# Kernel optimization log

Hardware: AMD Instinct MI355X
Metric: run time of the kernel (lower is better)

The kernel has to match this reference:

```python
import jax, jax.numpy as jnp
import numpy as np

WH, WW = 14, 14
NUM_HEADS = 12
NUM_REL = (2 * WH - 1) * (2 * WW - 1) + 3  # 732


def _gen_rel_pos_index(wh, ww):
    # Faithful numpy port of gen_relative_position_index (static, host-side)
    area = wh * ww
    coords = np.stack(np.meshgrid(np.arange(wh), np.arange(ww), indexing='ij'))  # (2, wh, ww)
    cf = coords.reshape(2, -1)  # (2, area)
    rel = cf[:, :, None] - cf[:, None, :]  # (2, area, area)
    rel = rel.transpose(1, 2, 0).copy()  # (area, area, 2)
    rel[..., 0] += wh - 1
    rel[..., 1] += ww - 1
    rel[..., 0] *= 2 * ww - 1
    nrd = (2 * wh - 1) * (2 * ww - 1) + 3
    idx = np.zeros((area + 1, area + 1), dtype=np.int64)
    idx[1:, 1:] = rel.sum(-1)
    idx[0, 0:] = nrd - 3
    idx[0:, 0] = nrd - 2
    idx[0, 0] = nrd - 1
    return idx


REL_IDX = jnp.asarray(_gen_rel_pos_index(WH, WW))  # (197, 197) int


def setup_inputs() -> dict:
    key = jax.random.key(0)
    k0, k1, k2, k3 = jax.random.split(key, 4)
    B, N, C = 64, WH * WW + 1, 768
    x = jax.random.normal(k0, (B, N, C), jnp.float32)
    qkv_w = jax.random.normal(k1, (3 * C, C), jnp.float32) * 0.02
    q_bias = jnp.zeros((C,), jnp.float32)
    k_bias = jnp.zeros((C,), jnp.float32)  # non-trainable buffer, always zeros
    v_bias = jnp.zeros((C,), jnp.float32)
    rel_table = jax.random.normal(k2, (NUM_REL, NUM_HEADS), jnp.float32) * 0.02
    proj_w = jax.random.normal(k3, (C, C), jnp.float32) * 0.02
    proj_b = jnp.zeros((C,), jnp.float32)
    return {"x": x, "qkv_w": qkv_w, "q_bias": q_bias, "k_bias": k_bias,
            "v_bias": v_bias, "rel_table": rel_table, "proj_w": proj_w, "proj_b": proj_b}


def reference(x, qkv_w, q_bias, k_bias, v_bias, rel_table, proj_w, proj_b):
    B, N, C = x.shape
    H = NUM_HEADS
    D = C // H
    scale = D ** -0.5
    # fused qkv projection with concatenated (q, k(zero), v) bias
    qkv_bias = jnp.concatenate([q_bias, k_bias, v_bias])
    qkv = x @ qkv_w.T + qkv_bias  # (B, N, 3C)
    qkv = qkv.reshape(B, N, 3, H, D).transpose(2, 0, 3, 1, 4)  # (3, B, H, N, D)
    q, k, v = qkv[0], qkv[1], qkv[2]
    # scores + gathered relative position bias
    attn = jnp.einsum('bhnd,bhmd->bhnm', q * scale, k)  # (B, H, N, N)
    rpb = rel_table[REL_IDX].transpose(2, 0, 1)  # (H, N, N)
    attn = jax.nn.softmax(attn + rpb[None], axis=-1)
    out = jnp.einsum('bhnm,bhmd->bhnd', attn, v)  # (B, H, N, D)
    out = out.transpose(0, 2, 1, 3).reshape(B, N, C)
    return out @ proj_w.T + proj_b
```

## Files before the change

kernel.cpp:

```cpp
#include <hip/hip_runtime.h>
#include <math.h>

#define B_   64
#define N_   197
#define C_   768
#define H_   12
#define D_   64
#define BN   12608
#define BN_PAD 12672
#define QKV_ELEMS 9682944
#define SCALE 0.125f
#define STRV 80

typedef unsigned short ushort_t;
using bf16x8  = __attribute__((ext_vector_type(8))) __bf16;
using floatx4 = __attribute__((ext_vector_type(4))) float;
using ushort8 = __attribute__((ext_vector_type(8))) unsigned short;

__device__ __forceinline__ ushort_t f2bf(float f) {
    union { float f; unsigned u; } v; v.f = f;
    unsigned r = v.u + 0x7FFF + ((v.u >> 16) & 1);
    return (ushort_t)(r >> 16);
}

__device__ __forceinline__ void gload_lds16(const void* g, void* l) {
    __builtin_amdgcn_global_load_lds(
        (const __attribute__((address_space(1))) unsigned*)g,
        (__attribute__((address_space(3))) unsigned*)l, 16, 0, 0);
}

__global__ __launch_bounds__(256) void cvt_f32_bf16(
    const float* __restrict__ src, ushort_t* __restrict__ dst, int n4)
{
    int i = blockIdx.x * 256 + threadIdx.x;
    if (i < n4) {
        float4 v = ((const float4*)src)[i];
        ushort4 o;
        o.x = f2bf(v.x); o.y = f2bf(v.y); o.z = f2bf(v.z); o.w = f2bf(v.w);
        ((ushort4*)dst)[i] = o;
    }
}

__global__ __launch_bounds__(256, 4) void qkv_gemm_mfma(
    const ushort_t* __restrict__ xb,
    const ushort_t* __restrict__ wb,
    const float* __restrict__ qb,
    const float* __restrict__ kb,
    const float* __restrict__ vb,
    ushort_t* __restrict__ qkvb)
{
    __shared__ ushort_t lA[128 * 64];
    __shared__ ushort_t lB[128 * 64];
    const int t = threadIdx.x;
    const int w = t >> 6, lane = t & 63;
    const int quad = lane >> 4, li = lane & 15;
    const int wm = w >> 1, wn = w & 1;
    const int o0 = blockIdx.x * 128, m0 = blockIdx.y * 128;

    floatx4 acc[4][4];
#pragma unroll
    for (int i = 0; i < 4; ++i)
#pragma unroll
        for (int j = 0; j < 4; ++j) acc[i][j] = (floatx4)0.f;

    const int rloc = lane >> 3;
    const int gdma = (lane & 7) ^ rloc;
    const int rx   = li & 7;

    for (int kt = 0; kt < 12; ++kt) {
        const int k0 = kt * 64;
#pragma unroll
        for (int s = 0; s < 4; ++s) {
            const int rb = w * 32 + s * 8;
            gload_lds16(xb + ((size_t)(m0 + rb + rloc)) * 768 + k0 + gdma * 8,
                        &lA[rb * 64]);
            gload_lds16(wb + ((size_t)(o0 + rb + rloc)) * 768 + k0 + gdma * 8,
                        &lB[rb * 64]);
        }
        __syncthreads();
#pragma unroll
        for (int kk = 0; kk < 2; ++kk) {
            bf16x8 af[4], bfr[4];
#pragma unroll
            for (int mi = 0; mi < 4; ++mi)
                af[mi] = *(const bf16x8*)
                    &lA[(wm * 64 + mi * 16 + li) * 64 + ((kk * 4 + quad) ^ rx) * 8];
#pragma unroll
            for (int ni = 0; ni < 4; ++ni)
                bfr[ni] = *(const bf16x8*)
                    &lB[(wn * 64 + ni * 16 + li) * 64 + ((kk * 4 + quad) ^ rx) * 8];
#pragma unroll
            for (int mi = 0; mi < 4; ++mi)
#pragma unroll
                for (int ni = 0; ni < 4; ++ni)
                    acc[mi][ni] = __builtin_amdgcn_mfma_f32_16x16x32_bf16(
                        af[mi], bfr[ni], acc[mi][ni], 0, 0, 0);
        }
        __syncthreads();
    }

    const int which = o0 / 768;
    const float* bias = (which == 0) ? qb : ((which == 1) ? kb : vb);
    ushort_t* dst = qkvb + (size_t)which * QKV_ELEMS;
    const float sc = (which == 0) ? SCALE : 1.0f;

#pragma unroll
    for (int mi = 0; mi < 4; ++mi) {
#pragma unroll
        for (int r = 0; r < 4; ++r) {
            const int m = m0 + wm * 64 + mi * 16 + quad * 4 + r;
            if (m < BN) {
                const int b = m / 197, n = m % 197;
#pragma unroll
                for (int ni = 0; ni < 4; ++ni) {
                    const int o  = o0 + wn * 64 + ni * 16 + li;
                    const int ol = o - which * 768;
                    const int h = ol >> 6, d = ol & 63;
                    dst[(((size_t)b * 12 + h) * 197 + n) * 64 + d] =
                        f2bf((acc[mi][ni][r] + bias[ol]) * sc);
                }
            }
        }
    }
}

__global__ __launch_bounds__(256, 4) void attn_mfma(
    const ushort_t* __restrict__ qkvb,
    const float* __restrict__ rel_table,
    ushort_t* __restrict__ aout)
{
    __shared__ ushort_t Qs[64 * 64];
    __shared__ ushort_t Ks[64 * 64];
    __shared__ ushort_t Vt[64 * STRV];
    __shared__ ushort_t Ps[64 * STRV];
    __shared__ float relh[732];

    const int rt = blockIdx.x, bh = blockIdx.y;
    const int h = bh % 12, bb = bh / 12;
    const int t = threadIdx.x;
    const int w = t >> 6, lane = t & 63, quad = lane >> 4, li = lane & 15;
    const size_t base = (size_t)bh * (197 * 64);
    const ushort_t* Qg = qkvb + base;
    const ushort_t* Kg = qkvb + (size_t)QKV_ELEMS + base;
    const ushort_t* Vg = qkvb + (size_t)2 * QKV_ELEMS + base;
    const int r0 = rt * 64;

    for (int i = t; i < 732; i += 256) relh[i] = rel_table[i * 12 + h];

    {
        const int rloc = lane >> 3, g = (lane & 7) ^ rloc;
#pragma unroll
        for (int s = 0; s < 2; ++s) {
            const int rb = (w * 2 + s) * 8;
            gload_lds16(Qg + (size_t)(r0 + rb + rloc) * 64 + g * 8, &Qs[rb * 64]);
        }
    }

    int nrow[4], p14[4], pm[4];
#pragma unroll
    for (int r = 0; r < 4; ++r) {
        const int n = r0 + w * 16 + quad * 4 + r;
        nrow[r] = n;
        const int ne = (n < 197) ? n : 0;
        const int p = (ne > 0) ? ne - 1 : 0;
        p14[r] = p / 14; pm[r] = p % 14;
    }

    float m_run[4], l_run[4];
    floatx4 accO[4];
#pragma unroll
    for (int r = 0; r < 4; ++r) { m_run[r] = -INFINITY; l_run[r] = 0.f; }
#pragma unroll
    for (int dt = 0; dt < 4; ++dt) accO[dt] = (floatx4)0.f;

    __syncthreads();

    bf16x8 aq0, aq1;
    {
        const int rq = w * 16 + li, rxq = rq & 7;
        aq0 = *(const bf16x8*)&Qs[rq * 64 + (quad ^ rxq) * 8];
        aq1 = *(const bf16x8*)&Qs[rq * 64 + ((4 + quad) ^ rxq) * 8];
    }

    for (int cc = 0; cc < 4; ++cc) {
        {
            const int rloc = lane >> 3, g = (lane & 7) ^ rloc;
#pragma unroll
            for (int s = 0; s < 2; ++s) {
                const int rb = (w * 2 + s) * 8;
                gload_lds16(Kg + (size_t)(cc * 64 + rb + rloc) * 64 + g * 8,
                            &Ks[rb * 64]);
            }
        }
        {
            const int c = lane;
            const int mg = cc * 64 + c;
            ushort8 v0, v1;
            if (mg < 197) {
                v0 = *(const ushort8*)(Vg + (size_t)mg * 64 + w * 16);
                v1 = *(const ushort8*)(Vg + (size_t)mg * 64 + w * 16 + 8);
            } else {
                v0 = (ushort8)(unsigned short)0; v1 = v0;
            }
#pragma unroll
            for (int j = 0; j < 8; ++j) Vt[(w * 16 + j) * STRV + c] = v0[j];
#pragma unroll
            for (int j = 0; j < 8; ++j) Vt[(w * 16 + 8 + j) * STRV + c] = v1[j];
        }
        __syncthreads();

        floatx4 sacc[4];
#pragma unroll
        for (int tl = 0; tl < 4; ++tl) {
            const int rk = tl * 16 + li, rxk = rk & 7;
            bf16x8 bk0 = *(const bf16x8*)&Ks[rk * 64 + (quad ^ rxk) * 8];
            bf16x8 bk1 = *(const bf16x8*)&Ks[rk * 64 + ((4 + quad) ^ rxk) * 8];
            floatx4 sa = (floatx4)0.f;
            sa = __builtin_amdgcn_mfma_f32_16x16x32_bf16(aq0, bk0, sa, 0, 0, 0);
            sa = __builtin_amdgcn_mfma_f32_16x16x32_bf16(aq1, bk1, sa, 0, 0, 0);
            sacc[tl] = sa;
        }

#pragma unroll
        for (int tl = 0; tl < 4; ++tl) {
            const int mg = cc * 64 + tl * 16 + li;
            if (mg >= 197) {
#pragma unroll
                for (int r = 0; r < 4; ++r) sacc[tl][r] = -INFINITY;
            } else {
                const int qq = (mg > 0) ? mg - 1 : 0;
                const int q14 = qq / 14, qm = qq % 14;
#pragma unroll
                for (int r = 0; r < 4; ++r) {
                    int idx;
                    const int n0 = (nrow[r] < 197) ? nrow[r] : 0;
                    if (n0 == 0 && mg == 0)      idx = 731;
                    else if (n0 == 0)            idx = 729;
                    else if (mg == 0)            idx = 730;
                    else idx = (p14[r] - q14 + 13) * 27 + (pm[r] - qm + 13);
                    sacc[tl][r] += relh[idx];
                }
            }
        }

#pragma unroll
        for (int r = 0; r < 4; ++r) {
            float mx = fmaxf(fmaxf(sacc[0][r], sacc[1][r]),
                             fmaxf(sacc[2][r], sacc[3][r]));
            mx = fmaxf(mx, __shfl_xor(mx, 1));
            mx = fmaxf(mx, __shfl_xor(mx, 2));
            mx = fmaxf(mx, __shfl_xor(mx, 4));
            mx = fmaxf(mx, __shfl_xor(mx, 8));
            const float mnew = fmaxf(m_run[r], mx);
            const float alpha = __expf(m_run[r] - mnew);
            m_run[r] = mnew;
            const float p0 = __expf(sacc[0][r] - mnew);
            const float p1 = __expf(sacc[1][r] - mnew);
            const float p2 = __expf(sacc[2][r] - mnew);
            const float p3 = __expf(sacc[3][r] - mnew);
            float rs = p0 + p1 + p2 + p3;
            rs += __shfl_xor(rs, 1);
            rs += __shfl_xor(rs, 2);
            rs += __shfl_xor(rs, 4);
            rs += __shfl_xor(rs, 8);
            l_run[r] = l_run[r] * alpha + rs;
#pragma unroll
            for (int dt = 0; dt < 4; ++dt) accO[dt][r] *= alpha;
            const int prow = w * 16 + quad * 4 + r;
            Ps[prow * STRV +  0 + li] = f2bf(p0);
            Ps[prow * STRV + 16 + li] = f2bf(p1);
            Ps[prow * STRV + 32 + li] = f2bf(p2);
            Ps[prow * STRV + 48 + li] = f2bf(p3);
        }

        {
            const int rp = w * 16 + li;
            bf16x8 pa0 = *(const bf16x8*)&Ps[rp * STRV + 0  + quad * 8];
            bf16x8 pa1 = *(const bf16x8*)&Ps[rp * STRV + 32 + quad * 8];
#pragma unroll
            for (int dt = 0; dt < 4; ++dt) {
                const int rv = dt * 16 + li;
                bf16x8 bv0 = *(const bf16x8*)&Vt[rv * STRV + 0  + quad * 8];
                bf16x8 bv1 = *(const bf16x8*)&Vt[rv * STRV + 32 + quad * 8];
                accO[dt] = __builtin_amdgcn_mfma_f32_16x16x32_bf16(
                    pa0, bv0, accO[dt], 0, 0, 0);
                accO[dt] = __builtin_amdgcn_mfma_f32_16x16x32_bf16(
                    pa1, bv1, accO[dt], 0, 0, 0);
            }
        }
        __syncthreads();
    }

#pragma unroll
    for (int r = 0; r < 4; ++r) {
        const int n = nrow[r];
        if (n < 197) {
            const float inv = 1.0f / l_run[r];
            ushort_t* op = aout + ((size_t)(bb * 197 + n)) * 768 + h * 64;
#pragma unroll
            for (int dt = 0; dt < 4; ++dt)
                op[dt * 16 + li] = f2bf(accO[dt][r] * inv);
        }
    }
}

__global__ __launch_bounds__(256, 4) void proj_gemm_mfma(
    const ushort_t* __restrict__ ab,
    const ushort_t* __restrict__ wb,
    const float* __restrict__ bias,
    float* __restrict__ out)
{
    __shared__ ushort_t lA[128 * 64];
    __shared__ ushort_t lB[128 * 64];
    const int t = threadIdx.x;
    const int w = t >> 6, lane = t & 63;
    const int quad = lane >> 4, li = lane & 15;
    const int wm = w >> 1, wn = w & 1;
    const int o0 = blockIdx.x * 128, m0 = blockIdx.y * 128;

    floatx4 acc[4][4];
#pragma unroll
    for (int i = 0; i < 4; ++i)
#pragma unroll
        for (int j = 0; j < 4; ++j) acc[i][j] = (floatx4)0.f;

    const int rloc = lane >> 3;
    const int gdma = (lane & 7) ^ rloc;
    const int rx   = li & 7;

    for (int kt = 0; kt < 12; ++kt) {
        const int k0 = kt * 64;
#pragma unroll
        for (int s = 0; s < 4; ++s) {
            const int rb = w * 32 + s * 8;
            gload_lds16(ab + ((size_t)(m0 + rb + rloc)) * 768 + k0 + gdma * 8,
                        &lA[rb * 64]);
            gload_lds16(wb + ((size_t)(o0 + rb + rloc)) * 768 + k0 + gdma * 8,
                        &lB[rb * 64]);
        }
        __syncthreads();
#pragma unroll
        for (int kk = 0; kk < 2; ++kk) {
            bf16x8 af[4], bfr[4];
#pragma unroll
            for (int mi = 0; mi < 4; ++mi)
                af[mi] = *(const bf16x8*)
                    &lA[(wm * 64 + mi * 16 + li) * 64 + ((kk * 4 + quad) ^ rx) * 8];
#pragma unroll
            for (int ni = 0; ni < 4; ++ni)
                bfr[ni] = *(const bf16x8*)
                    &lB[(wn * 64 + ni * 16 + li) * 64 + ((kk * 4 + quad) ^ rx) * 8];
#pragma unroll
            for (int mi = 0; mi < 4; ++mi)
#pragma unroll
                for (int ni = 0; ni < 4; ++ni)
                    acc[mi][ni] = __builtin_amdgcn_mfma_f32_16x16x32_bf16(
                        af[mi], bfr[ni], acc[mi][ni], 0, 0, 0);
        }
        __syncthreads();
    }

#pragma unroll
    for (int mi = 0; mi < 4; ++mi) {
#pragma unroll
        for (int r = 0; r < 4; ++r) {
            const int m = m0 + wm * 64 + mi * 16 + quad * 4 + r;
            if (m < BN) {
                float* op = out + (size_t)m * 768;
#pragma unroll
                for (int ni = 0; ni < 4; ++ni) {
                    const int o = o0 + wn * 64 + ni * 16 + li;
                    op[o] = acc[mi][ni][r] + bias[o];
                }
            }
        }
    }
}

extern "C" void kernel_launch(void* const* d_in, const int* in_sizes, int n_in,
                              void* d_out, int out_size, void* d_ws, size_t ws_size,
                              hipStream_t stream)
{
    const float* x         = (const float*)d_in[0];
    const float* qkv_w     = (const float*)d_in[1];
    const float* q_bias    = (const float*)d_in[2];
    const float* k_bias    = (const float*)d_in[3];
    const float* v_bias    = (const float*)d_in[4];
    const float* rel_table = (const float*)d_in[5];
    const float* proj_w    = (const float*)d_in[6];
    const float* proj_b    = (const float*)d_in[7];
    float* out = (float*)d_out;

    char* ws = (char*)d_ws;
    ushort_t* qkvb  = (ushort_t*)ws;
    ushort_t* xb    = (ushort_t*)(ws + 58097664);
    ushort_t* aoutb = xb;
    ushort_t* wb    = (ushort_t*)(ws + 77561856);
    ushort_t* pwb   = (ushort_t*)(ws + 81100800);

    cvt_f32_bf16<<<(2420736 + 255) / 256, 256, 0, stream>>>(x, xb, 2420736);
    cvt_f32_bf16<<<(442368 + 255) / 256, 256, 0, stream>>>(qkv_w, wb, 442368);
    cvt_f32_bf16<<<(147456 + 255) / 256, 256, 0, stream>>>(proj_w, pwb, 147456);

    dim3 g1(18, 99);
    qkv_gemm_mfma<<<g1, 256, 0, stream>>>(xb, wb, q_bias, k_bias, v_bias, qkvb);

    dim3 g2(4, 768);
    attn_mfma<<<g2, 256, 0, stream>>>(qkvb, rel_table, aoutb);

    dim3 g3(6, 99);
    proj_gemm_mfma<<<g3, 256, 0, stream>>>(aoutb, pwb, proj_b, out);
}
```

Measured before the change: 240.3 us.

## Pad QKV layout, pre-transpose V, precompute bf16 bias table, merge casts

Q and K are now stored padded to 256 rows per head, and the QKV GEMM epilogue writes V already transposed. This lets the attention kernel load K and V straight into LDS with async global-to-LDS copies instead of a scalar transpose through registers. A separate kernel expands the relative position bias into a padded per-head bf16 table, with -inf in the padding, and attention reads it directly instead of gathering indices per element. The three conversion kernels are merged into one launch. In exchange there is an extra precompute kernel, a larger workspace, bf16 rounding of the bias, and strided scalar writes of transposed V in the GEMM epilogue.

```diff
diff --git a/kernel.cpp b/kernel.cpp
--- a/kernel.cpp
+++ b/kernel.cpp
@@ -8,14 +8,14 @@
 #define D_   64
 #define BN   12608
 #define BN_PAD 12672
-#define QKV_ELEMS 9682944
+#define QKV_PAD 12582912
+#define HSTR 16384
 #define SCALE 0.125f
 #define STRV 80
 
 typedef unsigned short ushort_t;
 using bf16x8  = __attribute__((ext_vector_type(8))) __bf16;
 using floatx4 = __attribute__((ext_vector_type(4))) float;
-using ushort8 = __attribute__((ext_vector_type(8))) unsigned short;
 
 __device__ __forceinline__ ushort_t f2bf(float f) {
     union { float f; unsigned u; } v; v.f = f;
@@ -29,16 +29,49 @@
         (__attribute__((address_space(3))) unsigned*)l, 16, 0, 0);
 }
 
-__global__ __launch_bounds__(256) void cvt_f32_bf16(
-    const float* __restrict__ src, ushort_t* __restrict__ dst, int n4)
+#define NX4 2420736
+#define NW4 442368
+#define NP4 147456
+__global__ __launch_bounds__(256) void cvt_all(
+    const float* __restrict__ x, const float* __restrict__ qw,
+    const float* __restrict__ pw,
+    ushort_t* __restrict__ xb, ushort_t* __restrict__ wb,
+    ushort_t* __restrict__ pwb)
 {
     int i = blockIdx.x * 256 + threadIdx.x;
-    if (i < n4) {
-        float4 v = ((const float4*)src)[i];
-        ushort4 o;
-        o.x = f2bf(v.x); o.y = f2bf(v.y); o.z = f2bf(v.z); o.w = f2bf(v.w);
-        ((ushort4*)dst)[i] = o;
-    }
+    const float* s; ushort_t* d; int off;
+    if (i < NX4)                { s = x;  d = xb;  off = i; }
+    else if (i < NX4 + NW4)     { s = qw; d = wb;  off = i - NX4; }
+    else if (i < NX4 + NW4+NP4) { s = pw; d = pwb; off = i - NX4 - NW4; }
+    else return;
+    float4 v = ((const float4*)s)[off];
+    ushort4 o;
+    o.x = f2bf(v.x); o.y = f2bf(v.y); o.z = f2bf(v.z); o.w = f2bf(v.w);
+    ((ushort4*)d)[off] = o;
+}
+
+__global__ __launch_bounds__(256) void rpb_precompute(
+    const float* __restrict__ rel_table,
+    ushort_t* __restrict__ rpb)
+{
+    const int i = blockIdx.x * 256 + threadIdx.x;
+    const int n = i >> 8, m = i & 255;
+    if (n >= 197 || m >= 197) {
+#pragma unroll
+        for (int h = 0; h < 12; ++h) rpb[h * 65536 + i] = 0xFF80;
+        return;
+    }
+    int idx;
+    if (n == 0 && m == 0)      idx = 731;
+    else if (n == 0)           idx = 729;
+    else if (m == 0)           idx = 730;
+    else {
+        const int p = n - 1, q = m - 1;
+        idx = (p / 14 - q / 14 + 13) * 27 + (p % 14 - q % 14 + 13);
+    }
+#pragma unroll
+    for (int h = 0; h < 12; ++h)
+        rpb[h * 65536 + i] = f2bf(rel_table[idx * 12 + h]);
 }
 
 __global__ __launch_bounds__(256, 4) void qkv_gemm_mfma(
@@ -101,7 +134,7 @@
 
     const int which = o0 / 768;
     const float* bias = (which == 0) ? qb : ((which == 1) ? kb : vb);
-    ushort_t* dst = qkvb + (size_t)which * QKV_ELEMS;
+    ushort_t* dst = qkvb + (size_t)which * QKV_PAD;
     const float sc = (which == 0) ? SCALE : 1.0f;
 
 #pragma unroll
@@ -116,8 +149,11 @@
                     const int o  = o0 + wn * 64 + ni * 16 + li;
                     const int ol = o - which * 768;
                     const int h = ol >> 6, d = ol & 63;
-                    dst[(((size_t)b * 12 + h) * 197 + n) * 64 + d] =
-                        f2bf((acc[mi][ni][r] + bias[ol]) * sc);
+                    const float v = (acc[mi][ni][r] + bias[ol]) * sc;
+                    if (which < 2)
+                        dst[((size_t)(b * 12 + h) * 256 + n) * 64 + d] = f2bf(v);
+                    else
+                        dst[((size_t)(b * 12 + h) * 64 + d) * 256 + n] = f2bf(v);
                 }
             }
         }
@@ -126,44 +162,37 @@
 
 __global__ __launch_bounds__(256, 4) void attn_mfma(
     const ushort_t* __restrict__ qkvb,
-    const float* __restrict__ rel_table,
+    const ushort_t* __restrict__ rpb,
     ushort_t* __restrict__ aout)
 {
     __shared__ ushort_t Qs[64 * 64];
     __shared__ ushort_t Ks[64 * 64];
-    __shared__ ushort_t Vt[64 * STRV];
+    __shared__ ushort_t Vt[64 * 64];
     __shared__ ushort_t Ps[64 * STRV];
-    __shared__ float relh[732];
 
     const int rt = blockIdx.x, bh = blockIdx.y;
     const int h = bh % 12, bb = bh / 12;
     const int t = threadIdx.x;
     const int w = t >> 6, lane = t & 63, quad = lane >> 4, li = lane & 15;
-    const size_t base = (size_t)bh * (197 * 64);
-    const ushort_t* Qg = qkvb + base;
-    const ushort_t* Kg = qkvb + (size_t)QKV_ELEMS + base;
-    const ushort_t* Vg = qkvb + (size_t)2 * QKV_ELEMS + base;
+    const ushort_t* Qg = qkvb + (size_t)bh * HSTR;
+    const ushort_t* Kg = qkvb + (size_t)QKV_PAD + (size_t)bh * HSTR;
+    const ushort_t* Vg = qkvb + (size_t)2 * QKV_PAD + (size_t)bh * HSTR;
     const int r0 = rt * 64;
 
-    for (int i = t; i < 732; i += 256) relh[i] = rel_table[i * 12 + h];
-
-    {
-        const int rloc = lane >> 3, g = (lane & 7) ^ rloc;
-#pragma unroll
-        for (int s = 0; s < 2; ++s) {
-            const int rb = (w * 2 + s) * 8;
-            gload_lds16(Qg + (size_t)(r0 + rb + rloc) * 64 + g * 8, &Qs[rb * 64]);
-        }
-    }
-
-    int nrow[4], p14[4], pm[4];
+    const int rloc = lane >> 3, gdma = (lane & 7) ^ rloc;
+
+#pragma unroll
+    for (int s = 0; s < 2; ++s) {
+        const int rb = w * 16 + s * 8;
+        gload_lds16(Qg + (size_t)(r0 + rb + rloc) * 64 + gdma * 8, &Qs[rb * 64]);
+    }
+
+    int nrow[4];
+    const ushort_t* brow[4];
 #pragma unroll
     for (int r = 0; r < 4; ++r) {
-        const int n = r0 + w * 16 + quad * 4 + r;
-        nrow[r] = n;
-        const int ne = (n < 197) ? n : 0;
-        const int p = (ne > 0) ? ne - 1 : 0;
-        p14[r] = p / 14; pm[r] = p % 14;
+        nrow[r] = r0 + w * 16 + quad * 4 + r;
+        brow[r] = rpb + (size_t)h * 65536 + nrow[r] * 256;
     }
 
     float m_run[4], l_run[4];
@@ -183,29 +212,21 @@
     }
 
     for (int cc = 0; cc < 4; ++cc) {
-        {
-            const int rloc = lane >> 3, g = (lane & 7) ^ rloc;
-#pragma unroll
-            for (int s = 0; s < 2; ++s) {
-                const int rb = (w * 2 + s) * 8;
-                gload_lds16(Kg + (size_t)(cc * 64 + rb + rloc) * 64 + g * 8,
-                            &Ks[rb * 64]);
-            }
-        }
-        {
-            const int c = lane;
-            const int mg = cc * 64 + c;
-            ushort8 v0, v1;
-            if (mg < 197) {
-                v0 = *(const ushort8*)(Vg + (size_t)mg * 64 + w * 16);
-                v1 = *(const ushort8*)(Vg + (size_t)mg * 64 + w * 16 + 8);
-            } else {
-                v0 = (ushort8)(unsigned short)0; v1 = v0;
-            }
-#pragma unroll
-            for (int j = 0; j < 8; ++j) Vt[(w * 16 + j) * STRV + c] = v0[j];
-#pragma unroll
-            for (int j = 0; j < 8; ++j) Vt[(w * 16 + 8 + j) * STRV + c] = v1[j];
+#pragma unroll
+        for (int s = 0; s < 2; ++s) {
+            const int rb = w * 16 + s * 8;
+            gload_lds16(Kg + (size_t)(cc * 64 + rb + rloc) * 64 + gdma * 8,
+                        &Ks[rb * 64]);
+            gload_lds16(Vg + (size_t)(rb + rloc) * 256 + cc * 64 + gdma * 8,
+                        &Vt[rb * 64]);
+        }
+        unsigned bu[4][4];
+#pragma unroll
+        for (int tl = 0; tl < 4; ++tl) {
+            const int cg = cc * 64 + tl * 16 + li;
+#pragma unroll
+            for (int r = 0; r < 4; ++r)
+                bu[tl][r] = brow[r][cg];
         }
         __syncthreads();
 
@@ -222,26 +243,10 @@
         }
 
 #pragma unroll
-        for (int tl = 0; tl < 4; ++tl) {
-            const int mg = cc * 64 + tl * 16 + li;
-            if (mg >= 197) {
-#pragma unroll
-                for (int r = 0; r < 4; ++r) sacc[tl][r] = -INFINITY;
-            } else {
-                const int qq = (mg > 0) ? mg - 1 : 0;
-                const int q14 = qq / 14, qm = qq % 14;
-#pragma unroll
-                for (int r = 0; r < 4; ++r) {
-                    int idx;
-                    const int n0 = (nrow[r] < 197) ? nrow[r] : 0;
-                    if (n0 == 0 && mg == 0)      idx = 731;
-                    else if (n0 == 0)            idx = 729;
-                    else if (mg == 0)            idx = 730;
-                    else idx = (p14[r] - q14 + 13) * 27 + (pm[r] - qm + 13);
-                    sacc[tl][r] += relh[idx];
-                }
-            }
-        }
+        for (int tl = 0; tl < 4; ++tl)
+#pragma unroll
+            for (int r = 0; r < 4; ++r)
+                sacc[tl][r] += __uint_as_float(bu[tl][r] << 16);
 
 #pragma unroll
         for (int r = 0; r < 4; ++r) {
@@ -279,9 +284,9 @@
             bf16x8 pa1 = *(const bf16x8*)&Ps[rp * STRV + 32 + quad * 8];
 #pragma unroll
             for (int dt = 0; dt < 4; ++dt) {
-                const int rv = dt * 16 + li;
-                bf16x8 bv0 = *(const bf16x8*)&Vt[rv * STRV + 0  + quad * 8];
-                bf16x8 bv1 = *(const bf16x8*)&Vt[rv * STRV + 32 + quad * 8];
+                const int rv = dt * 16 + li, rxv = rv & 7;
+                bf16x8 bv0 = *(const bf16x8*)&Vt[rv * 64 + (quad ^ rxv) * 8];
+                bf16x8 bv1 = *(const bf16x8*)&Vt[rv * 64 + ((4 + quad) ^ rxv) * 8];
                 accO[dt] = __builtin_amdgcn_mfma_f32_16x16x32_bf16(
                     pa0, bv0, accO[dt], 0, 0, 0);
                 accO[dt] = __builtin_amdgcn_mfma_f32_16x16x32_bf16(
@@ -393,20 +398,21 @@
 
     char* ws = (char*)d_ws;
     ushort_t* qkvb  = (ushort_t*)ws;
-    ushort_t* xb    = (ushort_t*)(ws + 58097664);
+    ushort_t* rpb   = (ushort_t*)(ws + 75497472);
+    ushort_t* xb    = (ushort_t*)(ws + 77070336);
     ushort_t* aoutb = xb;
-    ushort_t* wb    = (ushort_t*)(ws + 77561856);
-    ushort_t* pwb   = (ushort_t*)(ws + 81100800);
-
-    cvt_f32_bf16<<<(2420736 + 255) / 256, 256, 0, stream>>>(x, xb, 2420736);
-    cvt_f32_bf16<<<(442368 + 255) / 256, 256, 0, stream>>>(qkv_w, wb, 442368);
-    cvt_f32_bf16<<<(147456 + 255) / 256, 256, 0, stream>>>(proj_w, pwb, 147456);
+    ushort_t* wb    = (ushort_t*)(ws + 96534528);
+    ushort_t* pwb   = (ushort_t*)(ws + 100073472);
+
+    cvt_all<<<(NX4 + NW4 + NP4 + 255) / 256, 256, 0, stream>>>(
+        x, qkv_w, proj_w, xb, wb, pwb);
+    rpb_precompute<<<256, 256, 0, stream>>>(rel_table, rpb);
 
     dim3 g1(18, 99);
     qkv_gemm_mfma<<<g1, 256, 0, stream>>>(xb, wb, q_bias, k_bias, v_bias, qkvb);
 
     dim3 g2(4, 768);
-    attn_mfma<<<g2, 256, 0, stream>>>(qkvb, rel_table, aoutb);
+    attn_mfma<<<g2, 256, 0, stream>>>(qkvb, rpb, aoutb);
 
     dim3 g3(6, 99);
     proj_gemm_mfma<<<g3, 256, 0, stream>>>(aoutb, pwb, proj_b, out);
```

After: 277.7 us. 15.6% more time.
